# Kernel optimization log

Hardware: AMD Instinct MI355X
Metric: run time of the kernel (lower is better)

Reference implementation:

```python
import jax, jax.numpy as jnp
import numpy as np

# config dims (see shape_source)
NO = 8        # Max_Object
NT = 32       # Max_Time
C = 512       # feat_dims
VD = 1024     # visual_dim
RD = 300      # self.nfeat (relation word-vector dim)
H = 4         # headnum
B = 8         # batch
No = NT * 2 * NO      # 512 object-graph nodes
Nr = NT * NO * NO     # 2048 relation-graph nodes


def _glorot(key, shape):
    fan_in = shape[0]
    return jax.random.normal(key, shape, dtype=jnp.float32) / np.sqrt(fan_in)


def setup_inputs() -> dict:
    key = jax.random.key(0)
    ks = jax.random.split(key, 18)
    inp = {
        "Ao": jax.random.uniform(ks[0], (B, No, No), dtype=jnp.float32),
        "srco": jax.random.normal(ks[1], (B, 1, 1, No, VD), dtype=jnp.float32),
        "Ar": jax.random.uniform(ks[2], (B, Nr, Nr), dtype=jnp.float32),
        "srcr": jax.random.normal(ks[3], (B, 1, 1, Nr, RD), dtype=jnp.float32),
        # GraphConvolution weights: gcl_o/gcl2_o and gcl_r/gcl2_r
        "Wo1": _glorot(ks[4], (VD, 1024)),
        "Wo2": _glorot(ks[5], (1024, C)),
        "Wr1": _glorot(ks[6], (RD, 1024)),
        "Wr2": _glorot(ks[7], (1024, C)),
        # MultiHeadAttention (e2n) projections
        "Wq": _glorot(ks[8], (C, C)), "bq": jnp.zeros((C,), jnp.float32),
        "Wk": _glorot(ks[9], (C, C)), "bk": jnp.zeros((C,), jnp.float32),
        "Wv": _glorot(ks[10], (C, C)), "bv": jnp.zeros((C,), jnp.float32),
        "Wp": _glorot(ks[11], (C, C)), "bp": jnp.zeros((C,), jnp.float32),
        # e2n_embed: Linear(2C -> C)
        "We": _glorot(ks[12], (2 * C, C)), "be": jnp.zeros((C,), jnp.float32),
    }
    return inp


def _gcn2(A, x, W1, W2):
    """Two stacked GraphConvolution layers with self-loops: relu((A+I) @ x @ W).
    A: (b,N,N), x: (b,N,Din). Vectorized over batch (torch code loops per-sample)."""
    eye = jnp.eye(A.shape[-1], dtype=A.dtype)
    Ah = A + eye
    h = jax.nn.relu(jnp.einsum('bij,bjd->bid', Ah, x @ W1))
    return jax.nn.relu(jnp.einsum('bij,bjd->bid', Ah, h @ W2))


def _mha(x, Wq, bq, Wk, bk, Wv, bv, Wp, bp):
    """Standard multi-head self-attention. x: (Bseg, S, C)."""
    Bs, S, _ = x.shape
    dh = C // H
    q = (x @ Wq + bq).reshape(Bs, S, H, dh)
    k = (x @ Wk + bk).reshape(Bs, S, H, dh)
    v = (x @ Wv + bv).reshape(Bs, S, H, dh)
    attn = jax.nn.softmax(jnp.einsum('bqhd,bkhd->bhqk', q, k) / np.sqrt(dh), axis=-1)
    o = jnp.einsum('bhqk,bkhd->bqhd', attn, v).reshape(Bs, S, C)
    return o @ Wp + bp


def _forward(Ao, srco, Ar, srcr, Wo1, Wo2, Wr1, Wr2,
             Wq, bq, Wk, bk, Wv, bv, Wp, bp, We, be):
    b = Ao.shape[0]
    # object-graph GCN (torch loops over batch; vectorized here)
    xo = srco[:, 0, 0, :, :VD]                       # (b, No, VD)
    srco_gcn = _gcn2(Ao, xo, Wo1, Wo2)               # (b, No, C)
    out_gcn_o = srco_gcn.reshape(b, NT, 2 * NO, C)
    # relation-graph GCN
    xr = srcr[:, 0, 0]                               # (b, Nr, RD)
    srcr_gcn = _gcn2(Ar, xr, Wr1, Wr2)               # (b, Nr, C)
    out_gcn_r = srcr_gcn.reshape(b, NT, NO * NO, C)
    # compute_e2n: segment-wise MHA over NO-token windows (torch loops over NO)
    r = out_gcn_r.reshape(b * NT, NO, NO, C)
    seg_a = r.reshape(b * NT * NO, NO, C)                      # rows of NOxNO grid
    a = _mha(seg_a, Wq, bq, Wk, bk, Wv, bv, Wp, bp).mean(axis=1)
    a = a.reshape(b * NT, NO, C)
    seg_o = jnp.swapaxes(r, 1, 2).reshape(b * NT * NO, NO, C)  # cols (permute 0,2,1,3)
    o = _mha(seg_o, Wq, bq, Wk, bk, Wv, bv, Wp, bp).mean(axis=1)
    o = o.reshape(b * NT, NO, C)
    tmp = jnp.concatenate([a, o], axis=1)                      # (b*NT, 2*NO, C)
    cat = jnp.concatenate([tmp, out_gcn_o.reshape(b * NT, 2 * NO, C)], axis=-1)
    out_e2n = cat @ We + be
    return out_e2n.reshape(b, NT, 2 * NO, C)


def reference(Ao, srco, Ar, srcr, Wo1, Wo2, Wr1, Wr2,
              Wq, bq, Wk, bk, Wv, bv, Wp, bp, We, be):
    return _forward(Ao, srco, Ar, srcr, Wo1, Wo2, Wr1, Wr2,
                    Wq, bq, Wk, bk, Wv, bv, Wp, bp, We, be)
```

## Files before the change

kernel.cpp:

```cpp
#include <hip/hip_runtime.h>
#include <hip/hip_bf16.h>


typedef __attribute__((ext_vector_type(4))) float f32x4;
typedef __attribute__((ext_vector_type(8))) short bf16x8s;

#define TILE 128
#define BKK 32
#define LDSS 40

__device__ inline void split2(float a, float b, unsigned& h, unsigned& l) {
    __hip_bfloat16 ha = __float2bfloat16(a), hb = __float2bfloat16(b);
    float ra = __bfloat162float(ha), rb = __bfloat162float(hb);
    __hip_bfloat16 la = __float2bfloat16(a - ra), lb = __float2bfloat16(b - rb);
    unsigned short uha = *(unsigned short*)&ha, uhb = *(unsigned short*)&hb;
    unsigned short ula = *(unsigned short*)&la, ulb = *(unsigned short*)&lb;
    h = (unsigned)uha | ((unsigned)uhb << 16);
    l = (unsigned)ula | ((unsigned)ulb << 16);
}

__device__ inline void splitw(float v, unsigned short& h, unsigned short& l) {
    __hip_bfloat16 hb = __float2bfloat16(v);
    __hip_bfloat16 lb = __float2bfloat16(v - __bfloat162float(hb));
    h = *(unsigned short*)&hb;
    l = *(unsigned short*)&lb;
}

__global__ __launch_bounds__(256) void gemm_asplit(
    const float* __restrict__ A, long long sA, int lda,
    const __hip_bfloat16* __restrict__ BTh, const __hip_bfloat16* __restrict__ BTl,
    long long sBT, int ldbt,
    __hip_bfloat16* __restrict__ Dh_, __hip_bfloat16* __restrict__ Dl_,
    long long sD, int ldd,
    const float* __restrict__ addN, long long sAddN, int ldaddN,
    const __hip_bfloat16* __restrict__ addTh, const __hip_bfloat16* __restrict__ addTl,
    long long sAddT, int ldaddT,
    int K, int relu)
{
    __shared__ __hip_bfloat16 Ah[TILE * LDSS], Al[TILE * LDSS];
    __shared__ __hip_bfloat16 Bh[TILE * LDSS], Bl[TILE * LDSS];

    const int tid  = threadIdx.x;
    const int lane = tid & 63;
    const int wave = tid >> 6;
    const int wm   = (wave >> 1) * 64;
    const int wn   = (wave & 1) * 64;
    const int row0 = blockIdx.y * TILE;
    const int col0 = blockIdx.x * TILE;
    const int b    = blockIdx.z;

    const float* Ab = A + (size_t)b * sA;
    const __hip_bfloat16* Bbh = BTh + (size_t)b * sBT;
    const __hip_bfloat16* Bbl = BTl + (size_t)b * sBT;

    f32x4 acc[4][4];
#pragma unroll
    for (int i = 0; i < 4; ++i)
#pragma unroll
        for (int j = 0; j < 4; ++j) acc[i][j] = (f32x4){0.f, 0.f, 0.f, 0.f};

    const int quad = lane >> 4;
    const int l16  = lane & 15;

    for (int k0 = 0; k0 < K; k0 += BKK) {
        __syncthreads();
#pragma unroll
        for (int it = 0; it < 2; ++it) {
            int task = tid + it * 256;
            int m = task >> 2, kq = task & 3;
            const float* ap = Ab + (size_t)(row0 + m) * lda + k0 + kq * 8;
            float4 v0 = *(const float4*)ap;
            float4 v1 = *(const float4*)(ap + 4);
            uint4 H, L;
            split2(v0.x, v0.y, H.x, L.x); split2(v0.z, v0.w, H.y, L.y);
            split2(v1.x, v1.y, H.z, L.z); split2(v1.z, v1.w, H.w, L.w);
            *(uint4*)(&Ah[m * LDSS + kq * 8]) = H;
            *(uint4*)(&Al[m * LDSS + kq * 8]) = L;
        }
#pragma unroll
        for (int it = 0; it < 2; ++it) {
            int task = tid + it * 256;
            int n = task >> 2, kq = task & 3;
            size_t off = (size_t)(col0 + n) * ldbt + k0 + kq * 8;
            *(uint4*)(&Bh[n * LDSS + kq * 8]) = *(const uint4*)(Bbh + off);
            *(uint4*)(&Bl[n * LDSS + kq * 8]) = *(const uint4*)(Bbl + off);
        }
        __syncthreads();

        bf16x8s ah[4], al[4], bh[4], bl[4];
#pragma unroll
        for (int mt = 0; mt < 4; ++mt) {
            int r = (wm + mt * 16 + l16) * LDSS + quad * 8;
            ah[mt] = *(const bf16x8s*)(&Ah[r]);
            al[mt] = *(const bf16x8s*)(&Al[r]);
        }
#pragma unroll
        for (int nt = 0; nt < 4; ++nt) {
            int r = (wn + nt * 16 + l16) * LDSS + quad * 8;
            bh[nt] = *(const bf16x8s*)(&Bh[r]);
            bl[nt] = *(const bf16x8s*)(&Bl[r]);
        }
#pragma unroll
        for (int mt = 0; mt < 4; ++mt)
#pragma unroll
            for (int nt = 0; nt < 4; ++nt) {
                acc[mt][nt] = __builtin_amdgcn_mfma_f32_16x16x32_bf16(ah[mt], bh[nt], acc[mt][nt], 0, 0, 0);
                acc[mt][nt] = __builtin_amdgcn_mfma_f32_16x16x32_bf16(ah[mt], bl[nt], acc[mt][nt], 0, 0, 0);
                acc[mt][nt] = __builtin_amdgcn_mfma_f32_16x16x32_bf16(al[mt], bh[nt], acc[mt][nt], 0, 0, 0);
            }
    }

    __hip_bfloat16* Dhb = Dh_ + (size_t)b * sD;
    __hip_bfloat16* Dlb = Dl_ + (size_t)b * sD;
    const float* AddN = addN ? addN + (size_t)b * sAddN : nullptr;
    const __hip_bfloat16* ATh = addTh ? addTh + (size_t)b * sAddT : nullptr;
    const __hip_bfloat16* ATl = addTl ? addTl + (size_t)b * sAddT : nullptr;
#pragma unroll
    for (int mt = 0; mt < 4; ++mt)
#pragma unroll
        for (int nt = 0; nt < 4; ++nt)
#pragma unroll
            for (int r = 0; r < 4; ++r) {
                int m = row0 + wm + mt * 16 + quad * 4 + r;
                int n = col0 + wn + nt * 16 + l16;
                float v = acc[mt][nt][r];
                if (AddN) v += AddN[(size_t)m * ldaddN + n];
                if (ATh) v += __bfloat162float(ATh[(size_t)n * ldaddT + m])
                            + __bfloat162float(ATl[(size_t)n * ldaddT + m]);
                if (relu && v < 0.f) v = 0.f;
                unsigned short hh, ll;
                splitw(v, hh, ll);
                size_t o = (size_t)m * ldd + n;
                *(unsigned short*)&Dhb[o] = hh;
                *(unsigned short*)&Dlb[o] = ll;
            }
}

__global__ __launch_bounds__(256) void gemm_planes(
    const __hip_bfloat16* __restrict__ Aph, const __hip_bfloat16* __restrict__ Apl,
    long long sA, int lda,
    const __hip_bfloat16* __restrict__ BTh, const __hip_bfloat16* __restrict__ BTl,
    long long sBT, int ldbt,
    void* __restrict__ D, __hip_bfloat16* __restrict__ Dl_, long long sD, int ldd,
    const float* __restrict__ bias,
    int K, int relu, int outMode)
{
    __shared__ __hip_bfloat16 Ah[TILE * LDSS], Al[TILE * LDSS];
    __shared__ __hip_bfloat16 Bh[TILE * LDSS], Bl[TILE * LDSS];

    const int tid  = threadIdx.x;
    const int lane = tid & 63;
    const int wave = tid >> 6;
    const int wm   = (wave >> 1) * 64;
    const int wn   = (wave & 1) * 64;
    const int row0 = blockIdx.y * TILE;
    const int col0 = blockIdx.x * TILE;
    const int b    = blockIdx.z;

    const __hip_bfloat16* Abh = Aph + (size_t)b * sA;
    const __hip_bfloat16* Abl = Apl + (size_t)b * sA;
    const __hip_bfloat16* Bbh = BTh + (size_t)b * sBT;
    const __hip_bfloat16* Bbl = BTl + (size_t)b * sBT;

    f32x4 acc[4][4];
#pragma unroll
    for (int i = 0; i < 4; ++i)
#pragma unroll
        for (int j = 0; j < 4; ++j) acc[i][j] = (f32x4){0.f, 0.f, 0.f, 0.f};

    const int quad = lane >> 4;
    const int l16  = lane & 15;

    for (int k0 = 0; k0 < K; k0 += BKK) {
        __syncthreads();
#pragma unroll
        for (int it = 0; it < 2; ++it) {
            int task = tid + it * 256;
            int m = task >> 2, kq = task & 3;
            size_t off = (size_t)(row0 + m) * lda + k0 + kq * 8;
            *(uint4*)(&Ah[m * LDSS + kq * 8]) = *(const uint4*)(Abh + off);
            *(uint4*)(&Al[m * LDSS + kq * 8]) = *(const uint4*)(Abl + off);
        }
#pragma unroll
        for (int it = 0; it < 2; ++it) {
            int task = tid + it * 256;
            int n = task >> 2, kq = task & 3;
            size_t off = (size_t)(col0 + n) * ldbt + k0 + kq * 8;
            *(uint4*)(&Bh[n * LDSS + kq * 8]) = *(const uint4*)(Bbh + off);
            *(uint4*)(&Bl[n * LDSS + kq * 8]) = *(const uint4*)(Bbl + off);
        }
        __syncthreads();

        bf16x8s ah[4], al[4], bh[4], bl[4];
#pragma unroll
        for (int mt = 0; mt < 4; ++mt) {
            int r = (wm + mt * 16 + l16) * LDSS + quad * 8;
            ah[mt] = *(const bf16x8s*)(&Ah[r]);
            al[mt] = *(const bf16x8s*)(&Al[r]);
        }
#pragma unroll
        for (int nt = 0; nt < 4; ++nt) {
            int r = (wn + nt * 16 + l16) * LDSS + quad * 8;
            bh[nt] = *(const bf16x8s*)(&Bh[r]);
            bl[nt] = *(const bf16x8s*)(&Bl[r]);
        }
#pragma unroll
        for (int mt = 0; mt < 4; ++mt)
#pragma unroll
            for (int nt = 0; nt < 4; ++nt) {
                acc[mt][nt] = __builtin_amdgcn_mfma_f32_16x16x32_bf16(ah[mt], bh[nt], acc[mt][nt], 0, 0, 0);
                acc[mt][nt] = __builtin_amdgcn_mfma_f32_16x16x32_bf16(ah[mt], bl[nt], acc[mt][nt], 0, 0, 0);
                acc[mt][nt] = __builtin_amdgcn_mfma_f32_16x16x32_bf16(al[mt], bh[nt], acc[mt][nt], 0, 0, 0);
            }
    }

    float* DbF = (float*)D + (size_t)b * sD;
    __hip_bfloat16* Dhb = (__hip_bfloat16*)D + (size_t)b * sD;
    __hip_bfloat16* Dlb = Dl_ ? Dl_ + (size_t)b * sD : nullptr;
#pragma unroll
    for (int mt = 0; mt < 4; ++mt)
#pragma unroll
        for (int nt = 0; nt < 4; ++nt)
#pragma unroll
            for (int r = 0; r < 4; ++r) {
                int m = row0 + wm + mt * 16 + quad * 4 + r;
                int n = col0 + wn + nt * 16 + l16;
                float v = acc[mt][nt][r];
                if (bias) v += bias[n];
                if (relu && v < 0.f) v = 0.f;
                if (outMode == 0) {
                    DbF[(size_t)m * ldd + n] = v;
                } else {
                    unsigned short hh, ll;
                    splitw(v, hh, ll);
                    size_t o = (size_t)m * ldd + n;
                    *(unsigned short*)&Dhb[o] = hh;
                    *(unsigned short*)&Dlb[o] = ll;
                }
            }
}

__global__ __launch_bounds__(256) void padtrans_split(
    const float* __restrict__ src,
    __hip_bfloat16* __restrict__ dsth, __hip_bfloat16* __restrict__ dstl,
    int R, int C, int Rp, int Cp)
{
    __shared__ float T[64][65];
    const int t = threadIdx.x;
    const int tr = t >> 4, tc = t & 15;
    const int c0 = blockIdx.x * 64, r0 = blockIdx.y * 64;
    const size_t bat = blockIdx.z;
    const float* sb = src + bat * (size_t)R * C;
    __hip_bfloat16* dhb = dsth + bat * (size_t)Cp * Rp;
    __hip_bfloat16* dlb = dstl + bat * (size_t)Cp * Rp;

#pragma unroll
    for (int i = 0; i < 4; ++i) {
        int rr = tr + i * 16;
        int gr = r0 + rr;
        float v0 = 0.f, v1 = 0.f, v2 = 0.f, v3 = 0.f;
        if (gr < R) {
            int c = c0 + tc * 4;
            const float* s = sb + (size_t)gr * C + c;
            if (c + 0 < C) v0 = s[0];
            if (c + 1 < C) v1 = s[1];
            if (c + 2 < C) v2 = s[2];
            if (c + 3 < C) v3 = s[3];
        }
        T[rr][tc * 4 + 0] = v0; T[rr][tc * 4 + 1] = v1;
        T[rr][tc * 4 + 2] = v2; T[rr][tc * 4 + 3] = v3;
    }
    __syncthreads();
#pragma unroll
    for (int i = 0; i < 4; ++i) {
        int cc = tr + i * 16;
        float4 v = { T[tc * 4 + 0][cc], T[tc * 4 + 1][cc],
                     T[tc * 4 + 2][cc], T[tc * 4 + 3][cc] };
        ushort4 H, L;
        splitw(v.x, H.x, L.x); splitw(v.y, H.y, L.y);
        splitw(v.z, H.z, L.z); splitw(v.w, H.w, L.w);
        size_t off = (size_t)(c0 + cc) * Rp + r0 + tc * 4;
        *(ushort4*)(dhb + off) = H;
        *(ushort4*)(dlb + off) = L;
    }
}

__global__ __launch_bounds__(256) void gemm_bf16(
    const __hip_bfloat16* __restrict__ A, long long sA, int lda,
    const __hip_bfloat16* __restrict__ B, long long sB, int ldb,
    void* __restrict__ D, long long sD, int ldd,
    const __hip_bfloat16* __restrict__ addsrc, long long sAdd, int ldadd,
    const float* __restrict__ bias,
    int K, int relu, int outF32)
{
    __shared__ __hip_bfloat16 As[TILE * LDSS];
    __shared__ __hip_bfloat16 Bs[TILE * LDSS];

    const int tid  = threadIdx.x;
    const int lane = tid & 63;
    const int wave = tid >> 6;
    const int wm   = (wave >> 1) * 64;
    const int wn   = (wave & 1) * 64;
    const int row0 = blockIdx.y * TILE;
    const int col0 = blockIdx.x * TILE;
    const int b    = blockIdx.z;

    const __hip_bfloat16* Ab = A + (size_t)b * sA;
    const __hip_bfloat16* Bb = B + (size_t)b * sB;

    f32x4 acc[4][4];
#pragma unroll
    for (int i = 0; i < 4; ++i)
#pragma unroll
        for (int j = 0; j < 4; ++j) acc[i][j] = (f32x4){0.f, 0.f, 0.f, 0.f};

    const int quad = lane >> 4;
    const int l16  = lane & 15;

    for (int k0 = 0; k0 < K; k0 += BKK) {
        __syncthreads();
#pragma unroll
        for (int it = 0; it < 2; ++it) {
            int task = tid + it * 256;
            int m = task >> 2, kq = task & 3;
            uint4 val = *(const uint4*)(Ab + (size_t)(row0 + m) * lda + k0 + kq * 8);
            *(uint4*)(&As[m * LDSS + kq * 8]) = val;
        }
#pragma unroll
        for (int it = 0; it < 2; ++it) {
            int task = tid + it * 256;
            int kk = task >> 4, n8 = task & 15;
            uint4 val = *(const uint4*)(Bb + (size_t)(k0 + kk) * ldb + col0 + n8 * 8);
            const __hip_bfloat16* v16 = (const __hip_bfloat16*)&val;
#pragma unroll
            for (int u = 0; u < 8; ++u)
                Bs[(n8 * 8 + u) * LDSS + kk] = v16[u];
        }
        __syncthreads();

        bf16x8s afrag[4], bfrag[4];
#pragma unroll
        for (int mt = 0; mt < 4; ++mt)
            afrag[mt] = *(const bf16x8s*)(&As[(wm + mt * 16 + l16) * LDSS + quad * 8]);
#pragma unroll
        for (int nt = 0; nt < 4; ++nt)
            bfrag[nt] = *(const bf16x8s*)(&Bs[(wn + nt * 16 + l16) * LDSS + quad * 8]);
#pragma unroll
        for (int mt = 0; mt < 4; ++mt)
#pragma unroll
            for (int nt = 0; nt < 4; ++nt)
                acc[mt][nt] = __builtin_amdgcn_mfma_f32_16x16x32_bf16(
                    afrag[mt], bfrag[nt], acc[mt][nt], 0, 0, 0);
    }

    __hip_bfloat16* Db16 = (__hip_bfloat16*)D + (size_t)b * sD;
    float*          DbF  = (float*)D + (size_t)b * sD;
    const __hip_bfloat16* Addb = addsrc ? addsrc + (size_t)b * sAdd : nullptr;
#pragma unroll
    for (int mt = 0; mt < 4; ++mt)
#pragma unroll
        for (int nt = 0; nt < 4; ++nt)
#pragma unroll
            for (int r = 0; r < 4; ++r) {
                int m = row0 + wm + mt * 16 + quad * 4 + r;
                int n = col0 + wn + nt * 16 + l16;
                float v = acc[mt][nt][r];
                if (Addb) v += __bfloat162float(Addb[(size_t)m * ldadd + n]);
                if (bias) v += bias[n];
                if (relu && v < 0.f) v = 0.f;
                if (outF32) DbF[(size_t)m * ldd + n] = v;
                else        Db16[(size_t)m * ldd + n] = __float2bfloat16(v);
            }
}

__global__ void convert_kernel(const float* __restrict__ src,
                               __hip_bfloat16* __restrict__ dst, int n4)
{
    int i = blockIdx.x * blockDim.x + threadIdx.x;
    if (i >= n4) return;
    float4 v = ((const float4*)src)[i];
    __hip_bfloat16 t0 = __float2bfloat16(v.x), t1 = __float2bfloat16(v.y);
    __hip_bfloat16 t2 = __float2bfloat16(v.z), t3 = __float2bfloat16(v.w);
    ushort4 o = { *(unsigned short*)&t0, *(unsigned short*)&t1,
                  *(unsigned short*)&t2, *(unsigned short*)&t3 };
    ((ushort4*)dst)[i] = o;
}

__global__ __launch_bounds__(256) void attn_kernel(
    const float* __restrict__ q,
    const float* __restrict__ k,
    const float* __restrict__ v,
    __hip_bfloat16* __restrict__ abar)
{
    __shared__ float qs[8][512], ks[8][512], vs[8][512];
    __shared__ float sc[4][8][8];
    __shared__ float wb[4][8];

    const int tid  = threadIdx.x;
    const int mode = blockIdx.y;
    const int g    = blockIdx.x >> 3;
    const int idx  = blockIdx.x & 7;
    const int rowBase = g * 64;

    for (int t = tid; t < 512; t += 256) {
        int p = t >> 6, c8 = (t & 63) * 8;
        int row = (mode == 0) ? (rowBase + idx * 8 + p) : (rowBase + p * 8 + idx);
        const float* qp = q + (size_t)row * 512 + c8;
        const float* kp = k + (size_t)row * 512 + c8;
        const float* vp = v + (size_t)row * 512 + c8;
        *(float4*)(&qs[p][c8])     = *(const float4*)(qp);
        *(float4*)(&qs[p][c8 + 4]) = *(const float4*)(qp + 4);
        *(float4*)(&ks[p][c8])     = *(const float4*)(kp);
        *(float4*)(&ks[p][c8 + 4]) = *(const float4*)(kp + 4);
        *(float4*)(&vs[p][c8])     = *(const float4*)(vp);
        *(float4*)(&vs[p][c8 + 4]) = *(const float4*)(vp + 4);
    }
    __syncthreads();

    {
        int h = tid >> 6, l = tid & 63;
        int i = l >> 3, j = l & 7;
        const float* qrow = &qs[i][h * 128];
        const float* krow = &ks[j][h * 128];
        float s = 0.f;
#pragma unroll
        for (int d = 0; d < 128; d += 4) {
            float4 qa = *(const float4*)(qrow + d);
            float4 kb = *(const float4*)(krow + d);
            s += qa.x * kb.x + qa.y * kb.y + qa.z * kb.z + qa.w * kb.w;
        }
        sc[h][i][j] = s * 0.08838834764831845f;
    }
    __syncthreads();

    if (tid < 32) {
        int h = tid >> 3, i = tid & 7;
        float mx = -1e30f;
#pragma unroll
        for (int j = 0; j < 8; ++j) mx = fmaxf(mx, sc[h][i][j]);
        float e[8], sum = 0.f;
#pragma unroll
        for (int j = 0; j < 8; ++j) { e[j] = __expf(sc[h][i][j] - mx); sum += e[j]; }
        float inv = 1.f / sum;
#pragma unroll
        for (int j = 0; j < 8; ++j) sc[h][i][j] = e[j] * inv;
    }
    __syncthreads();

    if (tid < 32) {
        int h = tid >> 3, j = tid & 7;
        float s = 0.f;
#pragma unroll
        for (int i = 0; i < 8; ++i) s += sc[h][i][j];
        wb[h][j] = s * 0.125f;
    }
    __syncthreads();

    {
        int orow = g * 16 + mode * 8 + idx;
        for (int c = tid; c < 512; c += 256) {
            int h = c >> 7;
            float o = 0.f;
#pragma unroll
            for (int j = 0; j < 8; ++j) o += wb[h][j] * vs[j][c];
            abar[(size_t)orow * 512 + c] = __float2bfloat16(o);
        }
    }
}


extern "C" void kernel_launch(void* const* d_in, const int* in_sizes, int n_in,
                              void* d_out, int out_size, void* d_ws, size_t ws_size,
                              hipStream_t stream)
{
    const float* Ao   = (const float*)d_in[0];
    const float* srco = (const float*)d_in[1];
    const float* Ar   = (const float*)d_in[2];
    const float* srcr = (const float*)d_in[3];
    const float* Wo1  = (const float*)d_in[4];
    const float* Wo2  = (const float*)d_in[5];
    const float* Wr1  = (const float*)d_in[6];
    const float* Wr2  = (const float*)d_in[7];
    const float* Wq   = (const float*)d_in[8];
    const float* bq   = (const float*)d_in[9];
    const float* Wk   = (const float*)d_in[10];
    const float* bk   = (const float*)d_in[11];
    const float* Wv   = (const float*)d_in[12];
    const float* bv   = (const float*)d_in[13];
    const float* Wp   = (const float*)d_in[14];
    const float* bp   = (const float*)d_in[15];
    const float* We   = (const float*)d_in[16];
    const float* be   = (const float*)d_in[17];
    float* out = (float*)d_out;

    char* ws = (char*)d_ws;
    const size_t R0 = 0;
    const size_t R1 = 67108864;
    const size_t R2 = 100663296;
    const size_t R3 = 134217728;
    const size_t R4 = 167772160;
    const size_t R5 = 192937984;

    __hip_bfloat16* HRh = (__hip_bfloat16*)(ws + R0);
    __hip_bfloat16* HRl = HRh + 16777216;
    float* qF   = (float*)(ws + R0);
    float* kF   = (float*)(ws + R0 + 33554432);
    float* T2Rf = (float*)(ws + R1);
    float* vF   = (float*)(ws + R1);
    __hip_bfloat16* Uh = (__hip_bfloat16*)(ws + R2);
    __hip_bfloat16* Ul = Uh + 6291456;
    __hip_bfloat16* T2RTh = (__hip_bfloat16*)(ws + R2);
    __hip_bfloat16* T2RTl = T2RTh + 8388608;
    __hip_bfloat16* GRh = (__hip_bfloat16*)(ws + R3);
    __hip_bfloat16* GRl = GRh + 8388608;
    __hip_bfloat16* XPTh = (__hip_bfloat16*)(ws + R4);
    __hip_bfloat16* XPTl = XPTh + 6291456;
    __hip_bfloat16* ABAR = (__hip_bfloat16*)(ws + R4);
    __hip_bfloat16* WPTh = (__hip_bfloat16*)(ws + R5);
    __hip_bfloat16* WPTl = WPTh + 327680;
    __hip_bfloat16* Wr2Th = (__hip_bfloat16*)(ws + R5 + 1310720);
    __hip_bfloat16* Wr2Tl = Wr2Th + 524288;
    __hip_bfloat16* WqTh = (__hip_bfloat16*)(ws + R5 + 3407872);
    __hip_bfloat16* WqTl = WqTh + 262144;
    __hip_bfloat16* WkTh = (__hip_bfloat16*)(ws + R5 + 4456448);
    __hip_bfloat16* WkTl = WkTh + 262144;
    __hip_bfloat16* WvTh = (__hip_bfloat16*)(ws + R5 + 5505024);
    __hip_bfloat16* WvTl = WvTh + 262144;

    __hip_bfloat16* TO    = (__hip_bfloat16*)(ws + R2 + 0);
    __hip_bfloat16* HO    = (__hip_bfloat16*)(ws + R2 + 8388608);
    __hip_bfloat16* T2O   = (__hip_bfloat16*)(ws + R2 + 16777216);
    __hip_bfloat16* CAT   = (__hip_bfloat16*)(ws + R2 + 20971520);
    __hip_bfloat16* srcoB = (__hip_bfloat16*)(ws + R2 + 29360128);
    __hip_bfloat16* AoB   = (__hip_bfloat16*)(ws + R2 + 37748736);
    __hip_bfloat16* Wo1B  = (__hip_bfloat16*)(ws + R2 + 41943040);
    __hip_bfloat16* Wo2B  = (__hip_bfloat16*)(ws + R2 + 44040192);
    __hip_bfloat16* WeB   = (__hip_bfloat16*)(ws + R2 + 45088768);
    __hip_bfloat16* WpB   = (__hip_bfloat16*)(ws + R2 + 46137344);

    dim3 blk(256);
    auto cvt = [&](const float* s, __hip_bfloat16* d, int n) {
        convert_kernel<<<dim3((n / 4 + 255) / 256), blk, 0, stream>>>(s, d, n / 4);
    };

    padtrans_split<<<dim3(6, 32, 8), blk, 0, stream>>>(srcr, XPTh, XPTl, 2048, 300, 2048, 384);
    padtrans_split<<<dim3(16, 5, 1), blk, 0, stream>>>(Wr1, WPTh, WPTl, 300, 1024, 320, 1024);
    padtrans_split<<<dim3(8, 16, 1), blk, 0, stream>>>(Wr2, Wr2Th, Wr2Tl, 1024, 512, 1024, 512);
    padtrans_split<<<dim3(8, 8, 1), blk, 0, stream>>>(Wq, WqTh, WqTl, 512, 512, 512, 512);
    padtrans_split<<<dim3(8, 8, 1), blk, 0, stream>>>(Wk, WkTh, WkTl, 512, 512, 512, 512);
    padtrans_split<<<dim3(8, 8, 1), blk, 0, stream>>>(Wv, WvTh, WvTl, 512, 512, 512, 512);

    gemm_asplit<<<dim3(3, 16, 8), blk, 0, stream>>>(
        Ar, 2048LL * 2048, 2048, XPTh, XPTl, 384LL * 2048, 2048,
        Uh, Ul, 2048LL * 384, 384,
        nullptr, 0, 0, XPTh, XPTl, 384LL * 2048, 2048,
        2048, 0);
    gemm_planes<<<dim3(8, 128, 1), blk, 0, stream>>>(
        Uh, Ul, 0, 384, WPTh, WPTl, 0, 320,
        HRh, HRl, 0, 1024, nullptr, 320, 1, 1);
    gemm_planes<<<dim3(4, 128, 1), blk, 0, stream>>>(
        HRh, HRl, 0, 1024, Wr2Th, Wr2Tl, 0, 1024,
        T2Rf, nullptr, 0, 512, nullptr, 1024, 0, 0);
    padtrans_split<<<dim3(8, 32, 8), blk, 0, stream>>>(T2Rf, T2RTh, T2RTl, 2048, 512, 2048, 512);
    gemm_asplit<<<dim3(4, 16, 8), blk, 0, stream>>>(
        Ar, 2048LL * 2048, 2048, T2RTh, T2RTl, 512LL * 2048, 2048,
        GRh, GRl, 2048LL * 512, 512,
        T2Rf, 2048LL * 512, 512, nullptr, nullptr, 0, 0,
        2048, 1);
    gemm_planes<<<dim3(4, 128, 1), blk, 0, stream>>>(
        GRh, GRl, 0, 512, WqTh, WqTl, 0, 512,
        qF, nullptr, 0, 512, bq, 512, 0, 0);
    gemm_planes<<<dim3(4, 128, 1), blk, 0, stream>>>(
        GRh, GRl, 0, 512, WkTh, WkTl, 0, 512,
        kF, nullptr, 0, 512, bk, 512, 0, 0);
    gemm_planes<<<dim3(4, 128, 1), blk, 0, stream>>>(
        GRh, GRl, 0, 512, WvTh, WvTl, 0, 512,
        vF, nullptr, 0, 512, bv, 512, 0, 0);
    attn_kernel<<<dim3(2048, 2), blk, 0, stream>>>(qF, kF, vF, ABAR);

    cvt(srco, srcoB, 4194304);
    cvt(Ao, AoB, 2097152);
    cvt(Wo1, Wo1B, 1048576);
    cvt(Wo2, Wo2B, 524288);
    cvt(We, WeB, 524288);
    cvt(Wp, WpB, 262144);
    gemm_bf16<<<dim3(8, 32, 1), blk, 0, stream>>>(srcoB, 0, 1024, Wo1B, 0, 1024,
        TO, 0, 1024, nullptr, 0, 0, nullptr, 1024, 0, 0);
    gemm_bf16<<<dim3(8, 4, 8), blk, 0, stream>>>(AoB, 512LL * 512, 512, TO, 512LL * 1024, 1024,
        HO, 512LL * 1024, 1024, TO, 512LL * 1024, 1024, nullptr, 512, 1, 0);
    gemm_bf16<<<dim3(4, 32, 1), blk, 0, stream>>>(HO, 0, 1024, Wo2B, 0, 512,
        T2O, 0, 512, nullptr, 0, 0, nullptr, 1024, 0, 0);
    gemm_bf16<<<dim3(4, 4, 8), blk, 0, stream>>>(AoB, 512LL * 512, 512, T2O, 512LL * 512, 512,
        (void*)(CAT + 512), 512LL * 1024, 1024, T2O, 512LL * 512, 512, nullptr, 512, 1, 0);
    gemm_bf16<<<dim3(4, 32, 1), blk, 0, stream>>>(ABAR, 0, 512, WpB, 0, 512,
        CAT, 0, 1024, nullptr, 0, 0, bp, 512, 0, 0);
    gemm_bf16<<<dim3(4, 32, 1), blk, 0, stream>>>(CAT, 0, 1024, WeB, 0, 512,
        out, 0, 512, nullptr, 0, 0, be, 1024, 0, 1);
}
```

Baseline: 1.203 ms.

## Pre-split Ar into bf16 planes, use direct global-to-LDS loads and block swizzle

Adds a split kernel that converts the large fp32 relation adjacency Ar into bf16 hi/lo planes once, so both relation-graph GEMMs can use the plane-based GEMM instead of re-splitting fp32 A tiles inside the kernel. The plane GEMM now loads tiles with global_load_lds into an XOR-swizzled, unpadded LDS layout, and gains fused add epilogues. A block-index swizzle is applied to both GEMM kernels to spread neighbouring tiles across XCDs. The new path needs extra workspace and an additional pass over Ar, and it only runs if the workspace is large enough.

```diff
diff --git a/kernel.cpp b/kernel.cpp
--- a/kernel.cpp
+++ b/kernel.cpp
@@ -8,6 +8,22 @@
 #define TILE 128
 #define BKK 32
 #define LDSS 40
+#define LDSL 32
+
+#if __has_builtin(__builtin_amdgcn_global_load_lds)
+#define HAVE_GLL 1
+#else
+#define HAVE_GLL 0
+#endif
+
+__device__ inline void gll16(const __hip_bfloat16* g, __hip_bfloat16* l) {
+#if HAVE_GLL
+    __builtin_amdgcn_global_load_lds(
+        (const __attribute__((address_space(1))) void*)g,
+        (__attribute__((address_space(3))) void*)l,
+        16, 0, 0);
+#endif
+}
 
 __device__ inline void split2(float a, float b, unsigned& h, unsigned& l) {
     __hip_bfloat16 ha = __float2bfloat16(a), hb = __float2bfloat16(b);
@@ -24,6 +40,149 @@
     __hip_bfloat16 lb = __float2bfloat16(v - __bfloat162float(hb));
     h = *(unsigned short*)&hb;
     l = *(unsigned short*)&lb;
+}
+
+__device__ inline void swz_block(int& bx, int& by, int& bz) {
+    int gx = gridDim.x, gy = gridDim.y;
+    int nwg = gx * gy * gridDim.z;
+    int flat = bx + gx * (by + gy * bz);
+    int cpx = nwg >> 3;
+    int w = (flat & 7) * cpx + (flat >> 3);
+    bx = w % gx;
+    int t = w / gx;
+    by = t % gy;
+    bz = t / gy;
+}
+
+__global__ __launch_bounds__(256) void gemm_planes(
+    const __hip_bfloat16* __restrict__ Aph, const __hip_bfloat16* __restrict__ Apl,
+    long long sA, int lda,
+    const __hip_bfloat16* __restrict__ BTh, const __hip_bfloat16* __restrict__ BTl,
+    long long sBT, int ldbt,
+    void* __restrict__ D, __hip_bfloat16* __restrict__ Dl_, long long sD, int ldd,
+    const float* __restrict__ addN, long long sAddN, int ldaddN,
+    const __hip_bfloat16* __restrict__ addTh, const __hip_bfloat16* __restrict__ addTl,
+    long long sAddT, int ldaddT,
+    const float* __restrict__ bias,
+    int K, int relu, int outMode)
+{
+    __shared__ __hip_bfloat16 Ah[TILE * LDSL], Al[TILE * LDSL];
+    __shared__ __hip_bfloat16 Bh[TILE * LDSL], Bl[TILE * LDSL];
+
+    int bx = blockIdx.x, by = blockIdx.y, bz = blockIdx.z;
+    swz_block(bx, by, bz);
+
+    const int tid  = threadIdx.x;
+    const int lane = tid & 63;
+    const int wave = tid >> 6;
+    const int wm   = (wave >> 1) * 64;
+    const int wn   = (wave & 1) * 64;
+    const int row0 = by * TILE;
+    const int col0 = bx * TILE;
+    const int b    = bz;
+
+    const __hip_bfloat16* Abh = Aph + (size_t)b * sA;
+    const __hip_bfloat16* Abl = Apl + (size_t)b * sA;
+    const __hip_bfloat16* Bbh = BTh + (size_t)b * sBT;
+    const __hip_bfloat16* Bbl = BTl + (size_t)b * sBT;
+
+    f32x4 acc[4][4];
+#pragma unroll
+    for (int i = 0; i < 4; ++i)
+#pragma unroll
+        for (int j = 0; j < 4; ++j) acc[i][j] = (f32x4){0.f, 0.f, 0.f, 0.f};
+
+    const int quad = lane >> 4;
+    const int l16  = lane & 15;
+
+    const int m0  = wave * 16 + (lane >> 2);
+    const int m1  = (wave + 4) * 16 + (lane >> 2);
+    const int sl  = lane & 3;
+    const int kq0 = sl ^ ((m0 >> 1) & 3);
+    const int kq1 = sl ^ ((m1 >> 1) & 3);
+    const size_t gA0 = (size_t)(row0 + m0) * lda + kq0 * 8;
+    const size_t gA1 = (size_t)(row0 + m1) * lda + kq1 * 8;
+    const size_t gB0 = (size_t)(col0 + m0) * ldbt + kq0 * 8;
+    const size_t gB1 = (size_t)(col0 + m1) * ldbt + kq1 * 8;
+    const int ldsc0 = wave * 512;
+    const int ldsc1 = (wave + 4) * 512;
+
+    for (int k0 = 0; k0 < K; k0 += BKK) {
+        __syncthreads();
+#if HAVE_GLL
+        gll16(Abh + gA0 + k0, &Ah[ldsc0]);
+        gll16(Abh + gA1 + k0, &Ah[ldsc1]);
+        gll16(Abl + gA0 + k0, &Al[ldsc0]);
+        gll16(Abl + gA1 + k0, &Al[ldsc1]);
+        gll16(Bbh + gB0 + k0, &Bh[ldsc0]);
+        gll16(Bbh + gB1 + k0, &Bh[ldsc1]);
+        gll16(Bbl + gB0 + k0, &Bl[ldsc0]);
+        gll16(Bbl + gB1 + k0, &Bl[ldsc1]);
+#else
+        *(uint4*)(&Ah[m0 * LDSL + sl * 8]) = *(const uint4*)(Abh + gA0 + k0);
+        *(uint4*)(&Ah[m1 * LDSL + sl * 8]) = *(const uint4*)(Abh + gA1 + k0);
+        *(uint4*)(&Al[m0 * LDSL + sl * 8]) = *(const uint4*)(Abl + gA0 + k0);
+        *(uint4*)(&Al[m1 * LDSL + sl * 8]) = *(const uint4*)(Abl + gA1 + k0);
+        *(uint4*)(&Bh[m0 * LDSL + sl * 8]) = *(const uint4*)(Bbh + gB0 + k0);
+        *(uint4*)(&Bh[m1 * LDSL + sl * 8]) = *(const uint4*)(Bbh + gB1 + k0);
+        *(uint4*)(&Bl[m0 * LDSL + sl * 8]) = *(const uint4*)(Bbl + gB0 + k0);
+        *(uint4*)(&Bl[m1 * LDSL + sl * 8]) = *(const uint4*)(Bbl + gB1 + k0);
+#endif
+        __syncthreads();
+
+        bf16x8s bhf[4], blf[4];
+#pragma unroll
+        for (int nt = 0; nt < 4; ++nt) {
+            int r = wn + nt * 16 + l16;
+            int ss = (quad ^ ((r >> 1) & 3)) * 8;
+            bhf[nt] = *(const bf16x8s*)(&Bh[r * LDSL + ss]);
+            blf[nt] = *(const bf16x8s*)(&Bl[r * LDSL + ss]);
+        }
+#pragma unroll
+        for (int mt = 0; mt < 4; ++mt) {
+            int r = wm + mt * 16 + l16;
+            int ss = (quad ^ ((r >> 1) & 3)) * 8;
+            bf16x8s ahf = *(const bf16x8s*)(&Ah[r * LDSL + ss]);
+            bf16x8s alf = *(const bf16x8s*)(&Al[r * LDSL + ss]);
+#pragma unroll
+            for (int nt = 0; nt < 4; ++nt) {
+                acc[mt][nt] = __builtin_amdgcn_mfma_f32_16x16x32_bf16(ahf, bhf[nt], acc[mt][nt], 0, 0, 0);
+                acc[mt][nt] = __builtin_amdgcn_mfma_f32_16x16x32_bf16(ahf, blf[nt], acc[mt][nt], 0, 0, 0);
+                acc[mt][nt] = __builtin_amdgcn_mfma_f32_16x16x32_bf16(alf, bhf[nt], acc[mt][nt], 0, 0, 0);
+            }
+        }
+    }
+
+    float* DbF = (float*)D + (size_t)b * sD;
+    __hip_bfloat16* Dhb = (__hip_bfloat16*)D + (size_t)b * sD;
+    __hip_bfloat16* Dlb = Dl_ ? Dl_ + (size_t)b * sD : nullptr;
+    const float* AddN = addN ? addN + (size_t)b * sAddN : nullptr;
+    const __hip_bfloat16* ATh = addTh ? addTh + (size_t)b * sAddT : nullptr;
+    const __hip_bfloat16* ATl = addTl ? addTl + (size_t)b * sAddT : nullptr;
+#pragma unroll
+    for (int mt = 0; mt < 4; ++mt)
+#pragma unroll
+        for (int nt = 0; nt < 4; ++nt)
+#pragma unroll
+            for (int r = 0; r < 4; ++r) {
+                int m = row0 + wm + mt * 16 + quad * 4 + r;
+                int n = col0 + wn + nt * 16 + l16;
+                float v = acc[mt][nt][r];
+                if (AddN) v += AddN[(size_t)m * ldaddN + n];
+                if (ATh) v += __bfloat162float(ATh[(size_t)n * ldaddT + m])
+                            + __bfloat162float(ATl[(size_t)n * ldaddT + m]);
+                if (bias) v += bias[n];
+                if (relu && v < 0.f) v = 0.f;
+                if (outMode == 0) {
+                    DbF[(size_t)m * ldd + n] = v;
+                } else {
+                    unsigned short hh, ll;
+                    splitw(v, hh, ll);
+                    size_t o = (size_t)m * ldd + n;
+                    *(unsigned short*)&Dhb[o] = hh;
+                    *(unsigned short*)&Dlb[o] = ll;
+                }
+            }
 }
 
 __global__ __launch_bounds__(256) void gemm_asplit(
@@ -136,110 +295,6 @@
             }
 }
 
-__global__ __launch_bounds__(256) void gemm_planes(
-    const __hip_bfloat16* __restrict__ Aph, const __hip_bfloat16* __restrict__ Apl,
-    long long sA, int lda,
-    const __hip_bfloat16* __restrict__ BTh, const __hip_bfloat16* __restrict__ BTl,
-    long long sBT, int ldbt,
-    void* __restrict__ D, __hip_bfloat16* __restrict__ Dl_, long long sD, int ldd,
-    const float* __restrict__ bias,
-    int K, int relu, int outMode)
-{
-    __shared__ __hip_bfloat16 Ah[TILE * LDSS], Al[TILE * LDSS];
-    __shared__ __hip_bfloat16 Bh[TILE * LDSS], Bl[TILE * LDSS];
-
-    const int tid  = threadIdx.x;
-    const int lane = tid & 63;
-    const int wave = tid >> 6;
-    const int wm   = (wave >> 1) * 64;
-    const int wn   = (wave & 1) * 64;
-    const int row0 = blockIdx.y * TILE;
-    const int col0 = blockIdx.x * TILE;
-    const int b    = blockIdx.z;
-
-    const __hip_bfloat16* Abh = Aph + (size_t)b * sA;
-    const __hip_bfloat16* Abl = Apl + (size_t)b * sA;
-    const __hip_bfloat16* Bbh = BTh + (size_t)b * sBT;
-    const __hip_bfloat16* Bbl = BTl + (size_t)b * sBT;
-
-    f32x4 acc[4][4];
-#pragma unroll
-    for (int i = 0; i < 4; ++i)
-#pragma unroll
-        for (int j = 0; j < 4; ++j) acc[i][j] = (f32x4){0.f, 0.f, 0.f, 0.f};
-
-    const int quad = lane >> 4;
-    const int l16  = lane & 15;
-
-    for (int k0 = 0; k0 < K; k0 += BKK) {
-        __syncthreads();
-#pragma unroll
-        for (int it = 0; it < 2; ++it) {
-            int task = tid + it * 256;
-            int m = task >> 2, kq = task & 3;
-            size_t off = (size_t)(row0 + m) * lda + k0 + kq * 8;
-            *(uint4*)(&Ah[m * LDSS + kq * 8]) = *(const uint4*)(Abh + off);
-            *(uint4*)(&Al[m * LDSS + kq * 8]) = *(const uint4*)(Abl + off);
-        }
-#pragma unroll
-        for (int it = 0; it < 2; ++it) {
-            int task = tid + it * 256;
-            int n = task >> 2, kq = task & 3;
-            size_t off = (size_t)(col0 + n) * ldbt + k0 + kq * 8;
-            *(uint4*)(&Bh[n * LDSS + kq * 8]) = *(const uint4*)(Bbh + off);
-            *(uint4*)(&Bl[n * LDSS + kq * 8]) = *(const uint4*)(Bbl + off);
-        }
-        __syncthreads();
-
-        bf16x8s ah[4], al[4], bh[4], bl[4];
-#pragma unroll
-        for (int mt = 0; mt < 4; ++mt) {
-            int r = (wm + mt * 16 + l16) * LDSS + quad * 8;
-            ah[mt] = *(const bf16x8s*)(&Ah[r]);
-            al[mt] = *(const bf16x8s*)(&Al[r]);
-        }
-#pragma unroll
-        for (int nt = 0; nt < 4; ++nt) {
-            int r = (wn + nt * 16 + l16) * LDSS + quad * 8;
-            bh[nt] = *(const bf16x8s*)(&Bh[r]);
-            bl[nt] = *(const bf16x8s*)(&Bl[r]);
-        }
-#pragma unroll
-        for (int mt = 0; mt < 4; ++mt)
-#pragma unroll
-            for (int nt = 0; nt < 4; ++nt) {
-                acc[mt][nt] = __builtin_amdgcn_mfma_f32_16x16x32_bf16(ah[mt], bh[nt], acc[mt][nt], 0, 0, 0);
-                acc[mt][nt] = __builtin_amdgcn_mfma_f32_16x16x32_bf16(ah[mt], bl[nt], acc[mt][nt], 0, 0, 0);
-                acc[mt][nt] = __builtin_amdgcn_mfma_f32_16x16x32_bf16(al[mt], bh[nt], acc[mt][nt], 0, 0, 0);
-            }
-    }
-
-    float* DbF = (float*)D + (size_t)b * sD;
-    __hip_bfloat16* Dhb = (__hip_bfloat16*)D + (size_t)b * sD;
-    __hip_bfloat16* Dlb = Dl_ ? Dl_ + (size_t)b * sD : nullptr;
-#pragma unroll
-    for (int mt = 0; mt < 4; ++mt)
-#pragma unroll
-        for (int nt = 0; nt < 4; ++nt)
-#pragma unroll
-            for (int r = 0; r < 4; ++r) {
-                int m = row0 + wm + mt * 16 + quad * 4 + r;
-                int n = col0 + wn + nt * 16 + l16;
-                float v = acc[mt][nt][r];
-                if (bias) v += bias[n];
-                if (relu && v < 0.f) v = 0.f;
-                if (outMode == 0) {
-                    DbF[(size_t)m * ldd + n] = v;
-                } else {
-                    unsigned short hh, ll;
-                    splitw(v, hh, ll);
-                    size_t o = (size_t)m * ldd + n;
-                    *(unsigned short*)&Dhb[o] = hh;
-                    *(unsigned short*)&Dlb[o] = ll;
-                }
-            }
-}
-
 __global__ __launch_bounds__(256) void padtrans_split(
     const float* __restrict__ src,
     __hip_bfloat16* __restrict__ dsth, __hip_bfloat16* __restrict__ dstl,
@@ -296,14 +351,17 @@
     __shared__ __hip_bfloat16 As[TILE * LDSS];
     __shared__ __hip_bfloat16 Bs[TILE * LDSS];
 
+    int bx = blockIdx.x, by = blockIdx.y, bz = blockIdx.z;
+    swz_block(bx, by, bz);
+
     const int tid  = threadIdx.x;
     const int lane = tid & 63;
     const int wave = tid >> 6;
     const int wm   = (wave >> 1) * 64;
     const int wn   = (wave & 1) * 64;
-    const int row0 = blockIdx.y * TILE;
-    const int col0 = blockIdx.x * TILE;
-    const int b    = blockIdx.z;
+    const int row0 = by * TILE;
+    const int col0 = bx * TILE;
+    const int b    = bz;
 
     const __hip_bfloat16* Ab = A + (size_t)b * sA;
     const __hip_bfloat16* Bb = B + (size_t)b * sB;
@@ -384,6 +442,20 @@
     ushort4 o = { *(unsigned short*)&t0, *(unsigned short*)&t1,
                   *(unsigned short*)&t2, *(unsigned short*)&t3 };
     ((ushort4*)dst)[i] = o;
+}
+
+__global__ void split_kernel(const float* __restrict__ src,
+                             __hip_bfloat16* __restrict__ dh,
+                             __hip_bfloat16* __restrict__ dl, int n4)
+{
+    int i = blockIdx.x * blockDim.x + threadIdx.x;
+    if (i >= n4) return;
+    float4 v = ((const float4*)src)[i];
+    ushort4 H, L;
+    splitw(v.x, H.x, L.x); splitw(v.y, H.y, L.y);
+    splitw(v.z, H.z, L.z); splitw(v.w, H.w, L.w);
+    ((ushort4*)dh)[i] = H;
+    ((ushort4*)dl)[i] = L;
 }
 
 __global__ __launch_bounds__(256) void attn_kernel(
@@ -500,6 +572,7 @@
     const size_t R3 = 134217728;
     const size_t R4 = 167772160;
     const size_t R5 = 192937984;
+    const size_t R6 = 199491584;
 
     __hip_bfloat16* HRh = (__hip_bfloat16*)(ws + R0);
     __hip_bfloat16* HRl = HRh + 16777216;
@@ -526,6 +599,9 @@
     __hip_bfloat16* WkTl = WkTh + 262144;
     __hip_bfloat16* WvTh = (__hip_bfloat16*)(ws + R5 + 5505024);
     __hip_bfloat16* WvTl = WvTh + 262144;
+    __hip_bfloat16* Arh = (__hip_bfloat16*)(ws + R6);
+    __hip_bfloat16* Arl = Arh + 33554432;
+    const bool haveArPlanes = ws_size >= R6 + 2ull * 67108864ull;
 
     __hip_bfloat16* TO    = (__hip_bfloat16*)(ws + R2 + 0);
     __hip_bfloat16* HO    = (__hip_bfloat16*)(ws + R2 + 8388608);
@@ -550,32 +626,59 @@
     padtrans_split<<<dim3(8, 8, 1), blk, 0, stream>>>(Wk, WkTh, WkTl, 512, 512, 512, 512);
     padtrans_split<<<dim3(8, 8, 1), blk, 0, stream>>>(Wv, WvTh, WvTl, 512, 512, 512, 512);
 
-    gemm_asplit<<<dim3(3, 16, 8), blk, 0, stream>>>(
-        Ar, 2048LL * 2048, 2048, XPTh, XPTl, 384LL * 2048, 2048,
-        Uh, Ul, 2048LL * 384, 384,
-        nullptr, 0, 0, XPTh, XPTl, 384LL * 2048, 2048,
-        2048, 0);
+    if (haveArPlanes) {
+        split_kernel<<<dim3(32768), blk, 0, stream>>>(Ar, Arh, Arl, 8388608);
+        gemm_planes<<<dim3(3, 16, 8), blk, 0, stream>>>(
+            Arh, Arl, 2048LL * 2048, 2048, XPTh, XPTl, 384LL * 2048, 2048,
+            Uh, Ul, 2048LL * 384, 384,
+            nullptr, 0, 0, XPTh, XPTl, 384LL * 2048, 2048,
+            nullptr, 2048, 0, 1);
+    } else {
+        gemm_asplit<<<dim3(3, 16, 8), blk, 0, stream>>>(
+            Ar, 2048LL * 2048, 2048, XPTh, XPTl, 384LL * 2048, 2048,
+            Uh, Ul, 2048LL * 384, 384,
+            nullptr, 0, 0, XPTh, XPTl, 384LL * 2048, 2048,
+            2048, 0);
+    }
     gemm_planes<<<dim3(8, 128, 1), blk, 0, stream>>>(
         Uh, Ul, 0, 384, WPTh, WPTl, 0, 320,
-        HRh, HRl, 0, 1024, nullptr, 320, 1, 1);
+        HRh, HRl, 0, 1024,
+        nullptr, 0, 0, nullptr, nullptr, 0, 0,
+        nullptr, 320, 1, 1);
     gemm_planes<<<dim3(4, 128, 1), blk, 0, stream>>>(
         HRh, HRl, 0, 1024, Wr2Th, Wr2Tl, 0, 1024,
-        T2Rf, nullptr, 0, 512, nullptr, 1024, 0, 0);
+        T2Rf, nullptr, 0, 512,
+        nullptr, 0, 0, nullptr, nullptr, 0, 0,
+        nullptr, 1024, 0, 0);
     padtrans_split<<<dim3(8, 32, 8), blk, 0, stream>>>(T2Rf, T2RTh, T2RTl, 2048, 512, 2048, 512);
-    gemm_asplit<<<dim3(4, 16, 8), blk, 0, stream>>>(
-        Ar, 2048LL * 2048, 2048, T2RTh, T2RTl, 512LL * 2048, 2048,
-        GRh, GRl, 2048LL * 512, 512,
-        T2Rf, 2048LL * 512, 512, nullptr, nullptr, 0, 0,
-        2048, 1);
+    if (haveArPlanes) {
+        gemm_planes<<<dim3(4, 16, 8), blk, 0, stream>>>(
+            Arh, Arl, 2048LL * 2048, 2048, T2RTh, T2RTl, 512LL * 2048, 2048,
+            GRh, GRl, 2048LL * 512, 512,
+            T2Rf, 2048LL * 512, 512, nullptr, nullptr, 0, 0,
+            nullptr, 2048, 1, 1);
+    } else {
+        gemm_asplit<<<dim3(4, 16, 8), blk, 0, stream>>>(
+            Ar, 2048LL * 2048, 2048, T2RTh, T2RTl, 512LL * 2048, 2048,
+            GRh, GRl, 2048LL * 512, 512,
+            T2Rf, 2048LL * 512, 512, nullptr, nullptr, 0, 0,
+            2048, 1);
+    }
     gemm_planes<<<dim3(4, 128, 1), blk, 0, stream>>>(
         GRh, GRl, 0, 512, WqTh, WqTl, 0, 512,
-        qF, nullptr, 0, 512, bq, 512, 0, 0);
+        qF, nullptr, 0, 512,
+        nullptr, 0, 0, nullptr, nullptr, 0, 0,
+        bq, 512, 0, 0);
     gemm_planes<<<dim3(4, 128, 1), blk, 0, stream>>>(
         GRh, GRl, 0, 512, WkTh, WkTl, 0, 512,
-        kF, nullptr, 0, 512, bk, 512, 0, 0);
+        kF, nullptr, 0, 512,
+        nullptr, 0, 0, nullptr, nullptr, 0, 0,
+        bk, 512, 0, 0);
     gemm_planes<<<dim3(4, 128, 1), blk, 0, stream>>>(
         GRh, GRl, 0, 512, WvTh, WvTl, 0, 512,
-        vF, nullptr, 0, 512, bv, 512, 0, 0);
+        vF, nullptr, 0, 512,
+        nullptr, 0, 0, nullptr, nullptr, 0, 0,
+        bv, 512, 0, 0);
     attn_kernel<<<dim3(2048, 2), blk, 0, stream>>>(qF, kF, vF, ABAR);
 
     cvt(srco, srcoB, 4194304);
```

Result: faster. 1.150 ms (-4.4%).
